# Optimization experiments

Hardware: AMD Instinct MI355X
Metric: run time of the kernel (lower is better)

Reference implementation:

```python
import jax, jax.numpy as jnp
import numpy as np

B, N_IN, D_IN, N_OUT, D_OUT, ROUTINGS = 512, 1152, 8, 10, 16, 3


def squash(s, axis=-1):
    # scale = |s|^2 / (1 + |s|^2) / (|s| + 1e-8)
    norm = jnp.linalg.norm(s, axis=axis, keepdims=True)
    return (norm ** 2 / (1.0 + norm ** 2) / (norm + 1e-8)) * s


def setup_inputs() -> dict:
    key = jax.random.key(0)
    k1, k2 = jax.random.split(key)
    x = jax.random.normal(k1, (B, N_IN, D_IN), dtype=jnp.float32)
    weight = 0.01 * jax.random.normal(k2, (N_OUT, N_IN, D_OUT, D_IN), dtype=jnp.float32)
    return {"x": x, "weight": weight}


def reference(x, weight):
    # x: [B, N_IN, D_IN]; weight: [N_OUT, N_IN, D_OUT, D_IN]
    # x_hat[b,o,n,:] = weight[o,n] @ x[b,n]  -> [B, N_OUT, N_IN, D_OUT]
    x_hat = jnp.einsum('onij,bnj->boni', weight, x)
    x_hat_det = jax.lax.stop_gradient(x_hat)

    # routing logits b: [B, N_OUT, N_IN]
    b = jnp.zeros(x_hat.shape[:3], dtype=x_hat.dtype)
    outputs = None
    for i in range(ROUTINGS):
        c = jax.nn.softmax(b, axis=1)  # softmax over output capsules
        if i == ROUTINGS - 1:
            outputs = squash(jnp.sum(c[..., None] * x_hat, axis=2))  # [B, N_OUT, D_OUT]
        else:
            outputs = squash(jnp.sum(c[..., None] * x_hat_det, axis=2))
            # agreement: b += <outputs, x_hat_det> over D_OUT
            b = b + jnp.einsum('bod,bond->bon', outputs, x_hat_det)
    return outputs  # [B, N_OUT, D_OUT]
```

## Files before the change

kernel.cpp:

```cpp
#include <hip/hip_runtime.h>
#include <hip/hip_bf16.h>
#include <hip/hip_fp16.h>

#define B_    512
#define NI    1152
#define NO    10
#define BT    16
#define NBT   32
#define NC    24
#define NCH   48
#define RNDS  6
#define RN    8

typedef __attribute__((ext_vector_type(8))) short bf16x8;
typedef __attribute__((ext_vector_type(4))) float f32x4;
typedef __attribute__((ext_vector_type(8))) unsigned short u16x8;

#define SPART_H    ((size_t)NC * NBT * NO * 256)
#define OUTSUM_F32 ((size_t)NBT * NO * 256)
#define XB_US      ((size_t)NBT * NC * RNDS * 1024)
#define WB_US      ((size_t)NC * RNDS * 12288)
#define WB2_US     ((size_t)NC * 12 * NO * 512)

__device__ inline unsigned short f2bf(float f) {
    __hip_bfloat16 h = __float2bfloat16(f);
    return *reinterpret_cast<unsigned short*>(&h);
}

__device__ __forceinline__ bf16x8 load_cvt8(const float* src) {
    f32x4 v0 = *reinterpret_cast<const f32x4*>(src);
    f32x4 v1 = *reinterpret_cast<const f32x4*>(src + 4);
    u16x8 u = { f2bf(v0[0]), f2bf(v0[1]), f2bf(v0[2]), f2bf(v0[3]),
                f2bf(v1[0]), f2bf(v1[1]), f2bf(v1[2]), f2bf(v1[3]) };
    return *reinterpret_cast<bf16x8*>(&u);
}

__device__ __forceinline__ void iter_epilogue(
    uint2 (*red)[NO * 64], const f32x4* sacc, float sc,
    int w, int l, int tid, unsigned short* base)
{
    #pragma unroll
    for (int o = 0; o < NO; ++o) {
        __half2 h01 = __floats2half2_rn(sacc[o][0] * sc, sacc[o][1] * sc);
        __half2 h23 = __floats2half2_rn(sacc[o][2] * sc, sacc[o][3] * sc);
        red[w][o * 64 + l] =
            make_uint2(*reinterpret_cast<unsigned int*>(&h01),
                       *reinterpret_cast<unsigned int*>(&h23));
    }
    __syncthreads();
    for (int g = tid; g < NO * 64; g += 256) {
        uint2 a0 = red[0][g], a1 = red[1][g], a2 = red[2][g], a3 = red[3][g];
        auto h2f2 = [](unsigned int u) {
            __half2 h = *reinterpret_cast<__half2*>(&u);
            return __half22float2(h);
        };
        float2 lo = h2f2(a0.x), l1 = h2f2(a1.x), l2 = h2f2(a2.x), l3 = h2f2(a3.x);
        float2 ho = h2f2(a0.y), h1 = h2f2(a1.y), h2 = h2f2(a2.y), h3 = h2f2(a3.y);
        float2 sl = { (lo.x + l1.x) + (l2.x + l3.x), (lo.y + l1.y) + (l2.y + l3.y) };
        float2 sh = { (ho.x + h1.x) + (h2.x + h3.x), (ho.y + h1.y) + (h2.y + h3.y) };
        __half2 p01 = __floats2half2_rn(sl.x, sl.y);
        __half2 p23 = __floats2half2_rn(sh.x, sh.y);
        *reinterpret_cast<uint2*>(base + (size_t)g * 4) =
            make_uint2(*reinterpret_cast<unsigned int*>(&p01),
                       *reinterpret_cast<unsigned int*>(&p23));
    }
}

__global__ __launch_bounds__(256) void cvt_xw(
    const float* __restrict__ x, const float* __restrict__ w,
    unsigned short* __restrict__ xb, unsigned short* __restrict__ wb,
    unsigned short* __restrict__ wb2)
{
    const int blk = blockIdx.x;
    if (blk < 2304) {
        const int t = blk * 256 + threadIdx.x;
        const int m   = t & 127;
        const int img = t >> 7;
        const int nl  = m >> 4, bl = m & 15;
        const int r   = img % RNDS;
        const int bc  = img / RNDS;
        const int nc  = bc % NC, bt = bc / NC;
        const int b   = bt * BT + bl;
        const int n   = nc * NCH + r * RN + nl;
        bf16x8 u = load_cvt8(x + ((size_t)b * NI + n) * 8);
        *reinterpret_cast<bf16x8*>(xb + (size_t)t * 8) = u;
    } else {
        const int t    = (blk - 2304) * 256 + threadIdx.x;
        const int lane = t & 63;
        const int gs   = (t >> 6) % 24;
        const int img  = t / 1536;
        const int h2   = lane >> 4, d = lane & 15;
        const int nl   = gs / 3, oq = gs % 3;
        const int r    = img % RNDS, nc = img / RNDS;
        const int o    = oq * 4 + h2;
        const int n    = nc * NCH + r * RN + nl;
        bf16x8 u = (bf16x8){0,0,0,0,0,0,0,0};
        if (o < NO) {
            u = load_cvt8(w + ((size_t)o * NI + n) * 128 + d * 8);
            const int g2  = r * 2 + (nl >> 2);
            const int hi2 = nl & 3;
            *reinterpret_cast<bf16x8*>(
                wb2 + (((size_t)nc * 12 + g2) * NO + o) * 512
                    + (hi2 * 16 + d) * 8) = u;
        }
        *reinterpret_cast<bf16x8*>(wb + (size_t)t * 8) = u;
    }
}

__global__ __launch_bounds__(256) void caps_it0(
    const unsigned short* __restrict__ xb,
    const unsigned short* __restrict__ wb2,
    unsigned short* __restrict__ s_part)
{
    __shared__ uint2 red[4][NO * 64];

    const int tid = threadIdx.x;
    const int wv  = tid >> 6;
    const int l   = tid & 63;
    const int b16 = l & 15;
    const int hi  = l >> 4;
    const int blk = blockIdx.x;
    const int xcd = blk & 7, idx = blk >> 3;
    const int nc  = xcd * 3 + (idx >> 5);
    const int bt  = idx & 31;

    f32x4 sacc[NO];
    #pragma unroll
    for (int o = 0; o < NO; ++o) sacc[o] = (f32x4){0.f, 0.f, 0.f, 0.f};

    const unsigned short* xbase = xb + (size_t)(bt * NC + nc) * (RNDS * 1024);
    const unsigned short* w2base = wb2 + (size_t)nc * (12 * NO * 512);

    #pragma unroll 1
    for (int gi = 0; gi < 3; ++gi) {
        const int g  = wv * 3 + gi;
        const int nn = 4 * g + hi;
        const int r  = nn >> 3, nl = nn & 7;
        bf16x8 bv4 = *reinterpret_cast<const bf16x8*>(
            xbase + (size_t)r * 1024 + (nl * 16 + b16) * 8);
        #pragma unroll
        for (int o = 0; o < NO; ++o) {
            bf16x8 av4 = *reinterpret_cast<const bf16x8*>(
                w2base + ((size_t)g * NO + o) * 512 + l * 8);
            sacc[o] = __builtin_amdgcn_mfma_f32_16x16x32_bf16(
                av4, bv4, sacc[o], 0, 0, 0);
        }
    }

    iter_epilogue(red, sacc, 0.1f, wv, l, tid,
                  s_part + ((size_t)nc * NBT + bt) * 2560);
}

__global__ __launch_bounds__(256, 3) void caps_itr(
    const unsigned short* __restrict__ xb,
    const unsigned short* __restrict__ wb,
    const float* __restrict__ outsum,
    unsigned short* __restrict__ s_part)
{
    __shared__ uint2 red[4][NO * 64];

    const int tid = threadIdx.x;
    const int wv  = tid >> 6;
    const int l   = tid & 63;
    const int b16 = l & 15;
    const int hi  = l >> 4;
    const int blk = blockIdx.x;
    const int xcd = blk & 7, idx = blk >> 3;
    const int nc  = xcd * 3 + (idx >> 5);
    const int bt  = idx & 31;

    f32x4 outf[NO];
    #pragma unroll
    for (int o = 0; o < NO; ++o)
        outf[o] = *reinterpret_cast<const f32x4*>(
            outsum + (((size_t)bt * NO + o) * 64 + l) * 4);

    f32x4 sacc[NO];
    #pragma unroll
    for (int o = 0; o < NO; ++o) sacc[o] = (f32x4){0.f, 0.f, 0.f, 0.f};

    const unsigned short* xbase = xb + (size_t)(bt * NC + nc) * (RNDS * 1024);
    const unsigned short* wbase = wb + (size_t)nc * (RNDS * 12288);

    #pragma unroll 1
    for (int r = 0; r < RNDS; ++r) {
        const unsigned short* xr = xbase + (size_t)r * 1024;
        const unsigned short* wr = wbase + (size_t)r * 12288;
        #pragma unroll 1
        for (int i = 0; i < 2; ++i) {
            const int nl = wv * 2 + i;
            bf16x8 bv = *reinterpret_cast<const bf16x8*>(
                xr + nl * 128 + b16 * 8);
            bf16x8 avv[3];
            #pragma unroll
            for (int oq = 0; oq < 3; ++oq)
                avv[oq] = *reinterpret_cast<const bf16x8*>(
                    wr + (nl * 3 + oq) * 512 + l * 8);
            bf16x8 bvt[4];
            #pragma unroll
            for (int t = 0; t < 4; ++t)
                bvt[t] = (hi == t) ? bv : (bf16x8){0,0,0,0,0,0,0,0};

            f32x4 xh[NO];
            float lg[NO];
            #pragma unroll
            for (int oq = 0; oq < 3; ++oq) {
                const int tmax = (oq < 2) ? 4 : 2;
                #pragma unroll
                for (int t = 0; t < tmax; ++t) {
                    const int o = oq * 4 + t;
                    xh[o] = __builtin_amdgcn_mfma_f32_16x16x32_bf16(
                        avv[oq], bvt[t], (f32x4){0.f, 0.f, 0.f, 0.f}, 0, 0, 0);
                    float pp = outf[o][0] * xh[o][0];
                    pp = fmaf(outf[o][1], xh[o][1], pp);
                    pp = fmaf(outf[o][2], xh[o][2], pp);
                    pp = fmaf(outf[o][3], xh[o][3], pp);
                    pp += __shfl_xor(pp, 16, 64);
                    pp += __shfl_xor(pp, 32, 64);
                    lg[o] = pp;
                }
            }
            float sum = 0.f;
            #pragma unroll
            for (int o = 0; o < NO; ++o) { lg[o] = __expf(lg[o]); sum += lg[o]; }
            const float rs = __builtin_amdgcn_rcpf(sum);
            #pragma unroll
            for (int o = 0; o < NO; ++o) {
                const float cc = lg[o] * rs;
                sacc[o][0] = fmaf(cc, xh[o][0], sacc[o][0]);
                sacc[o][1] = fmaf(cc, xh[o][1], sacc[o][1]);
                sacc[o][2] = fmaf(cc, xh[o][2], sacc[o][2]);
                sacc[o][3] = fmaf(cc, xh[o][3], sacc[o][3]);
            }
        }
    }

    iter_epilogue(red, sacc, 1.0f, wv, l, tid,
                  s_part + ((size_t)nc * NBT + bt) * 2560);
}

template<int MODE>
__global__ __launch_bounds__(256) void caps_squash(
    const unsigned short* __restrict__ s_part,
    float* __restrict__ outsum,
    float* __restrict__ dout)
{
    __shared__ float sq[256];
    const int bo = blockIdx.x;
    const int t  = threadIdx.x;

    float s = 0.f;
    #pragma unroll 4
    for (int nc = 0; nc < NC; ++nc) {
        __half h = *reinterpret_cast<const __half*>(
            s_part + ((size_t)nc * NBT * NO + bo) * 256 + t);
        s += __half2float(h);
    }

    float n2 = s * s;
    n2 += __shfl_xor(n2, 1, 64);
    n2 += __shfl_xor(n2, 2, 64);
    sq[t] = n2;
    __syncthreads();
    const int base = t & 63;
    n2 = (sq[base] + sq[64 + base]) + (sq[128 + base] + sq[192 + base]);

    const float norm  = sqrtf(n2);
    const float scale = n2 / ((1.f + n2) * (norm + 1e-8f));
    const float v = scale * s;

    if constexpr (MODE == 0) {
        outsum[(size_t)bo * 256 + t] = v;
    } else if constexpr (MODE == 1) {
        outsum[(size_t)bo * 256 + t] += v;
    } else {
        const int bt = bo / NO, o = bo - bt * NO;
        const int b16 = (t >> 2) & 15, hi = t >> 6, q = t & 3;
        dout[((size_t)(bt * BT + b16) * NO + o) * 16 + hi * 4 + q] = v;
    }
}

extern "C" void kernel_launch(void* const* d_in, const int* in_sizes, int n_in,
                              void* d_out, int out_size, void* d_ws, size_t ws_size,
                              hipStream_t stream) {
    const float* x = (const float*)d_in[0];
    const float* w = (const float*)d_in[1];
    float* out = (float*)d_out;

    unsigned short* s_part = (unsigned short*)d_ws;
    float*          outsum = (float*)(s_part + SPART_H);
    unsigned short* xb     = (unsigned short*)(outsum + OUTSUM_F32);
    unsigned short* wb     = xb + XB_US;
    unsigned short* wb2    = wb + WB_US;

    dim3 gI(NBT * NC), bI(256);
    dim3 gS(NBT * NO), bS(256);

    cvt_xw<<<dim3(3168), dim3(256), 0, stream>>>(x, w, xb, wb, wb2);
    caps_it0<<<gI, bI, 0, stream>>>(xb, wb2, s_part);
    caps_squash<0><<<gS, bS, 0, stream>>>(s_part, outsum, nullptr);
    caps_itr<<<gI, bI, 0, stream>>>(xb, wb, outsum, s_part);
    caps_squash<1><<<gS, bS, 0, stream>>>(s_part, outsum, nullptr);
    caps_itr<<<gI, bI, 0, stream>>>(xb, wb, outsum, s_part);
    caps_squash<2><<<gS, bS, 0, stream>>>(s_part, nullptr, out);
}
```

Baseline: 65.86 us.

## Prefetch next group's operands and recompute MFMA instead of holding x_hat registers

Flattens the round/sub-iteration loops into one loop and software-prefetches the next group's x and weight fragments into registers while the current group computes. It also stops keeping all ten x_hat MFMA results live across the softmax. Instead it reissues the MFMAs in a second pass to accumulate the weighted sums, which lowers register pressure. The cost is double the MFMA work per group and extra registers for the prefetched operands.

```diff
diff --git a/kernel.cpp b/kernel.cpp
--- a/kernel.cpp
+++ b/kernel.cpp
@@ -182,55 +182,71 @@
     const unsigned short* xbase = xb + (size_t)(bt * NC + nc) * (RNDS * 1024);
     const unsigned short* wbase = wb + (size_t)nc * (RNDS * 12288);
 
+    auto bvp = [&](int g) {
+        const int r = g >> 1, nl = wv * 2 + (g & 1);
+        return reinterpret_cast<const bf16x8*>(
+            xbase + (size_t)r * 1024 + nl * 128 + b16 * 8);
+    };
+    auto avp = [&](int g, int oq) {
+        const int r = g >> 1, nl = wv * 2 + (g & 1);
+        return reinterpret_cast<const bf16x8*>(
+            wbase + (size_t)r * 12288 + (nl * 3 + oq) * 512 + l * 8);
+    };
+
+    const bf16x8 zero = {0,0,0,0,0,0,0,0};
+    bf16x8 pb  = *bvp(0);
+    bf16x8 pa0 = *avp(0, 0), pa1 = *avp(0, 1), pa2 = *avp(0, 2);
+
     #pragma unroll 1
-    for (int r = 0; r < RNDS; ++r) {
-        const unsigned short* xr = xbase + (size_t)r * 1024;
-        const unsigned short* wr = wbase + (size_t)r * 12288;
-        #pragma unroll 1
-        for (int i = 0; i < 2; ++i) {
-            const int nl = wv * 2 + i;
-            bf16x8 bv = *reinterpret_cast<const bf16x8*>(
-                xr + nl * 128 + b16 * 8);
-            bf16x8 avv[3];
+    for (int g = 0; g < 2 * RNDS; ++g) {
+        bf16x8 cb = pb;
+        bf16x8 avv[3] = { pa0, pa1, pa2 };
+        if (g + 1 < 2 * RNDS) {
+            pb  = *bvp(g + 1);
+            pa0 = *avp(g + 1, 0);
+            pa1 = *avp(g + 1, 1);
+            pa2 = *avp(g + 1, 2);
+        }
+
+        float lg[NO];
+        #pragma unroll
+        for (int oq = 0; oq < 3; ++oq) {
+            const int tmax = (oq < 2) ? 4 : 2;
             #pragma unroll
-            for (int oq = 0; oq < 3; ++oq)
-                avv[oq] = *reinterpret_cast<const bf16x8*>(
-                    wr + (nl * 3 + oq) * 512 + l * 8);
-            bf16x8 bvt[4];
+            for (int t = 0; t < tmax; ++t) {
+                const int o = oq * 4 + t;
+                bf16x8 bvt = (hi == t) ? cb : zero;
+                f32x4 xh = __builtin_amdgcn_mfma_f32_16x16x32_bf16(
+                    avv[oq], bvt, (f32x4){0.f, 0.f, 0.f, 0.f}, 0, 0, 0);
+                float pp = outf[o][0] * xh[0];
+                pp = fmaf(outf[o][1], xh[1], pp);
+                pp = fmaf(outf[o][2], xh[2], pp);
+                pp = fmaf(outf[o][3], xh[3], pp);
+                pp += __shfl_xor(pp, 16, 64);
+                pp += __shfl_xor(pp, 32, 64);
+                lg[o] = pp;
+            }
+        }
+        float sum = 0.f;
+        #pragma unroll
+        for (int o = 0; o < NO; ++o) { lg[o] = __expf(lg[o]); sum += lg[o]; }
+        const float rs = __builtin_amdgcn_rcpf(sum);
+        #pragma unroll
+        for (int o = 0; o < NO; ++o) lg[o] *= rs;
+
+        #pragma unroll
+        for (int oq = 0; oq < 3; ++oq) {
+            const int tmax = (oq < 2) ? 4 : 2;
             #pragma unroll
-            for (int t = 0; t < 4; ++t)
-                bvt[t] = (hi == t) ? bv : (bf16x8){0,0,0,0,0,0,0,0};
-
-            f32x4 xh[NO];
-            float lg[NO];
-            #pragma unroll
-            for (int oq = 0; oq < 3; ++oq) {
-                const int tmax = (oq < 2) ? 4 : 2;
-                #pragma unroll
-                for (int t = 0; t < tmax; ++t) {
-                    const int o = oq * 4 + t;
-                    xh[o] = __builtin_amdgcn_mfma_f32_16x16x32_bf16(
-                        avv[oq], bvt[t], (f32x4){0.f, 0.f, 0.f, 0.f}, 0, 0, 0);
-                    float pp = outf[o][0] * xh[o][0];
-                    pp = fmaf(outf[o][1], xh[o][1], pp);
-                    pp = fmaf(outf[o][2], xh[o][2], pp);
-                    pp = fmaf(outf[o][3], xh[o][3], pp);
-                    pp += __shfl_xor(pp, 16, 64);
-                    pp += __shfl_xor(pp, 32, 64);
-                    lg[o] = pp;
-                }
-            }
-            float sum = 0.f;
-            #pragma unroll
-            for (int o = 0; o < NO; ++o) { lg[o] = __expf(lg[o]); sum += lg[o]; }
-            const float rs = __builtin_amdgcn_rcpf(sum);
-            #pragma unroll
-            for (int o = 0; o < NO; ++o) {
-                const float cc = lg[o] * rs;
-                sacc[o][0] = fmaf(cc, xh[o][0], sacc[o][0]);
-                sacc[o][1] = fmaf(cc, xh[o][1], sacc[o][1]);
-                sacc[o][2] = fmaf(cc, xh[o][2], sacc[o][2]);
-                sacc[o][3] = fmaf(cc, xh[o][3], sacc[o][3]);
+            for (int t = 0; t < tmax; ++t) {
+                const int o = oq * 4 + t;
+                bf16x8 bvt = (hi == t) ? cb : zero;
+                f32x4 xh = __builtin_amdgcn_mfma_f32_16x16x32_bf16(
+                    avv[oq], bvt, (f32x4){0.f, 0.f, 0.f, 0.f}, 0, 0, 0);
+                sacc[o][0] = fmaf(lg[o], xh[0], sacc[o][0]);
+                sacc[o][1] = fmaf(lg[o], xh[1], sacc[o][1]);
+                sacc[o][2] = fmaf(lg[o], xh[2], sacc[o][2]);
+                sacc[o][3] = fmaf(lg[o], xh[3], sacc[o][3]);
             }
         }
     }
```

Measured after the change: 66.30 us. No clear change (+0.7%).
